# Optimization experiments

Hardware: AMD Instinct MI355X
Metric: run time of the kernel (lower is better)

The kernel has to match this reference:

```python
import jax, jax.numpy as jnp
import numpy as np

N_NODES = 50000

def _gcn_conv(x, W, b, src, dst, num_nodes):
    # PyG GCNConv: linear transform, then D^{-1/2} A_hat D^{-1/2} aggregation (A_hat has self-loops).
    xw = x @ W                                   # [N, out]
    ones = jnp.ones(src.shape[0], dtype=x.dtype)
    deg = jax.ops.segment_sum(ones, dst, num_segments=num_nodes)  # in-degree incl. self loop
    dinv = jnp.where(deg > 0, jax.lax.rsqrt(deg), 0.0)
    norm = dinv[src] * dinv[dst]                 # [E]
    msg = xw[src] * norm[:, None]                # [E, out] gather + scale
    out = jax.ops.segment_sum(msg, dst, num_segments=num_nodes)   # scatter-add
    return out + b

def _add_self_loops(edge_index, num_nodes):
    loop = jnp.arange(num_nodes, dtype=edge_index.dtype)
    src = jnp.concatenate([edge_index[0], loop])
    dst = jnp.concatenate([edge_index[1], loop])
    return src, dst

def setup_inputs() -> dict:
    key = jax.random.key(0)
    k = jax.random.split(key, 6)
    in_dim, hid_dim, out_dim = 256, 128, 64
    n_edges = 800000
    x = jax.random.normal(k[0], (N_NODES, in_dim), dtype=jnp.float32)
    edge_index = jax.random.randint(k[1], (2, n_edges), 0, N_NODES, dtype=jnp.int64)
    W1 = jax.random.normal(k[2], (in_dim, hid_dim), dtype=jnp.float32) / np.sqrt(in_dim)
    b1 = jnp.zeros((hid_dim,), dtype=jnp.float32)
    W2 = jax.random.normal(k[3], (hid_dim, out_dim), dtype=jnp.float32) / np.sqrt(hid_dim)
    b2 = jnp.zeros((out_dim,), dtype=jnp.float32)
    return {"x": x, "edge_index": edge_index, "W1": W1, "b1": b1, "W2": W2, "b2": b2}

def reference(x, edge_index, W1, b1, W2, b2):
    src, dst = _add_self_loops(edge_index, N_NODES)
    h = jnp.tanh(_gcn_conv(x, W1, b1, src, dst, N_NODES))
    out = _gcn_conv(h, W2, b2, src, dst, N_NODES)
    return out
```

## Files before the change

### kernel.cpp

```cpp
#include <hip/hip_runtime.h>

#define INDIM 256
#define HID 128
#define OUTD 64
#define BINSHIFT 8
#define MAXBIN 256

typedef _Float16 f16x8 __attribute__((ext_vector_type(8)));
typedef float    f32x4 __attribute__((ext_vector_type(4)));

__global__ __launch_bounds__(256) void k_hist_setup(const int* __restrict__ dst, int* __restrict__ bin_counts,
                                                    int E,
                                                    const float* __restrict__ W1, const float* __restrict__ W2,
                                                    _Float16* __restrict__ W1t, _Float16* __restrict__ W2t) {
    __shared__ int h[MAXBIN];
    int tid = threadIdx.x;
    h[tid] = 0;
    __syncthreads();
    int base = blockIdx.x * 4096;
#pragma unroll
    for (int i = 0; i < 16; i++) {
        int e = base + i * 256 + tid;
        if (e < E) atomicAdd(&h[dst[e] >> BINSHIFT], 1);
    }
    __syncthreads();
    int v = h[tid];
    if (v) atomicAdd(&bin_counts[tid], v);

    constexpr int NW1 = HID * INDIM;
    constexpr int NW2 = OUTD * HID;
    int id = blockIdx.x * 256 + tid;
    if (id < NW1) {
        int n = id / INDIM, k = id % INDIM;
        W1t[id] = (_Float16)W1[k * HID + n];
    } else if (id < NW1 + NW2) {
        int j = id - NW1;
        int n = j / HID, k = j % HID;
        W2t[j] = (_Float16)W2[k * OUTD + n];
    }
}

__global__ __launch_bounds__(256) void k_bscan(const int* __restrict__ bin_counts,
                                               int* __restrict__ bin_start, int* __restrict__ bin_cursor,
                                               int* __restrict__ row_start, int NBIN, int M, int E) {
    __shared__ int s[256];
    int tid = threadIdx.x;
    int v = (tid < NBIN) ? bin_counts[tid] : 0;
    s[tid] = v;
    __syncthreads();
#pragma unroll
    for (int off = 1; off < 256; off <<= 1) {
        int t = (tid >= off) ? s[tid - off] : 0;
        __syncthreads();
        s[tid] += t;
        __syncthreads();
    }
    if (tid < NBIN) {
        int excl = s[tid] - v;
        bin_start[tid] = excl;
        bin_cursor[tid] = excl;
    }
    if (tid == 0) {
        bin_start[NBIN] = E;
        row_start[M] = E;
    }
}

__global__ __launch_bounds__(256) void k_binfill(const int* __restrict__ src, const int* __restrict__ dst,
                                                 int* __restrict__ bin_cursor, int* __restrict__ binned, int E) {
    __shared__ int h[MAXBIN];
    __shared__ int rb[MAXBIN];
    int tid = threadIdx.x;
    h[tid] = 0;
    __syncthreads();
    int base = blockIdx.x * 2048;
    int ep[8], eb[8], rk[8];
#pragma unroll
    for (int i = 0; i < 8; i++) {
        int e = base + i * 256 + tid;
        if (e < E) {
            int s = src[e], d = dst[e];
            ep[i] = (s << 8) | (d & 255);
            eb[i] = d >> BINSHIFT;
            rk[i] = atomicAdd(&h[eb[i]], 1);
        } else {
            eb[i] = -1;
        }
    }
    __syncthreads();
    int c = h[tid];
    if (c) rb[tid] = atomicAdd(&bin_cursor[tid], c);
    __syncthreads();
#pragma unroll
    for (int i = 0; i < 8; i++) {
        if (eb[i] >= 0) binned[rb[eb[i]] + rk[i]] = ep[i];
    }
}

__global__ __launch_bounds__(256) void k_csr(const int* __restrict__ binned, const int* __restrict__ bin_start,
                                             int* __restrict__ row_start, float* __restrict__ dinv,
                                             int* __restrict__ edge_src, int M) {
    __shared__ int cnt[256];
    __shared__ int s[256];
    __shared__ int cur[256];
    int b = blockIdx.x, tid = threadIdx.x;
    int beg = bin_start[b], end = bin_start[b + 1];
    cnt[tid] = 0;
    __syncthreads();
    for (int i = beg + tid; i < end; i += 256) {
        atomicAdd(&cnt[binned[i] & 255], 1);
    }
    __syncthreads();
    int c = cnt[tid];
    s[tid] = c;
    __syncthreads();
#pragma unroll
    for (int off = 1; off < 256; off <<= 1) {
        int t = (tid >= off) ? s[tid - off] : 0;
        __syncthreads();
        s[tid] += t;
        __syncthreads();
    }
    int start = beg + s[tid] - c;
    int node = (b << BINSHIFT) + tid;
    if (node < M) {
        row_start[node] = start;
        dinv[node] = rsqrtf(1.0f + (float)c);
    }
    cur[tid] = start;
    __syncthreads();
    for (int i = beg + tid; i < end; i += 256) {
        int p = binned[i];
        int pos = atomicAdd(&cur[p & 255], 1);
        edge_src[pos] = p >> 8;
    }
}

template <int BN, int K, typename AT>
__global__ __launch_bounds__(256) void k_gemm_mfma(
    const AT* __restrict__ X, const _Float16* __restrict__ Wt,
    const float* __restrict__ dinv, _Float16* __restrict__ XW16, int M)
{
    constexpr int BM = 64;
    constexpr int BK = 32;
    constexpr int NT = BN / 16;
    constexpr int LDK = BK + 8;

    __shared__ __align__(16) _Float16 As[BM][LDK];
    __shared__ __align__(16) _Float16 Bs[BN][LDK];

    const int tid  = threadIdx.x;
    const int wave = tid >> 6;
    const int lane = tid & 63;
    const int m    = lane & 15;
    const int q    = lane >> 4;
    const int rb   = blockIdx.x * BM;

    f32x4 acc[NT];
#pragma unroll
    for (int t = 0; t < NT; t++) acc[t] = (f32x4){0.f, 0.f, 0.f, 0.f};

    for (int kt = 0; kt < K; kt += BK) {
        if (kt) __syncthreads();
        if constexpr (sizeof(AT) == 4) {
#pragma unroll
            for (int i = 0; i < BM * 8 / 256; i++) {
                int ch  = tid + i * 256;
                int row = ch >> 3;
                int c4  = ch & 7;
                int gr  = rb + row;
                float4 v = make_float4(0.f, 0.f, 0.f, 0.f);
                if (gr < M) v = *(const float4*)((const float*)X + (long)gr * K + kt + c4 * 4);
                _Float16* p = &As[row][c4 * 4];
                p[0] = (_Float16)v.x; p[1] = (_Float16)v.y;
                p[2] = (_Float16)v.z; p[3] = (_Float16)v.w;
            }
        } else {
            int row = tid >> 2;
            int c8  = tid & 3;
            int gr  = rb + row;
            uint4 v = make_uint4(0u, 0u, 0u, 0u);
            if (gr < M) v = *(const uint4*)((const _Float16*)X + (long)gr * K + kt + c8 * 8);
            *(uint4*)(&As[row][c8 * 8]) = v;
        }
#pragma unroll
        for (int i = 0; i < BN * 8 / 256; i++) {
            int ch = tid + i * 256;
            int n  = ch >> 3;
            int c4 = ch & 7;
            *(ushort4*)(&Bs[n][c4 * 4]) =
                *(const ushort4*)(Wt + (long)n * K + kt + c4 * 4);
        }
        __syncthreads();

        f16x8 af = *(const f16x8*)(&As[wave * 16 + m][q * 8]);
#pragma unroll
        for (int t = 0; t < NT; t++) {
            f16x8 bf = *(const f16x8*)(&Bs[t * 16 + m][q * 8]);
            acc[t] = __builtin_amdgcn_mfma_f32_16x16x32_f16(af, bf, acc[t], 0, 0, 0);
        }
    }

    int row0 = rb + wave * 16 + q * 4;
#pragma unroll
    for (int r = 0; r < 4; r++) {
        int row = row0 + r;
        if (row < M) {
            float di = dinv[row];
#pragma unroll
            for (int t = 0; t < NT; t++) {
                XW16[(long)row * BN + t * 16 + m] = (_Float16)(acc[t][r] * di);
            }
        }
    }
}

template <int F, bool TANH, typename OutT>
__global__ __launch_bounds__(256) void k_agg_csr(const int* __restrict__ row_start,
                                                 const int* __restrict__ edge_src,
                                                 const _Float16* __restrict__ feat,
                                                 const float* __restrict__ bias,
                                                 const float* __restrict__ dinv,
                                                 OutT* __restrict__ out, int M) {
    constexpr int LPN = F / 8;
    constexpr int NPB = 256 / LPN;
    int n = blockIdx.x * NPB + threadIdx.x / LPN;
    int c = threadIdx.x % LPN;
    if (n >= M) return;
    int beg = row_start[n], end = row_start[n + 1];

    f16x8 self = *(const f16x8*)(feat + (long)n * F + c * 8);
    float acc[8], acc2[8];
#pragma unroll
    for (int k = 0; k < 8; k++) { acc[k] = (float)self[k]; acc2[k] = 0.f; }

    int j = beg;
    for (; j + 3 < end; j += 4) {
        int s0 = edge_src[j],     s1 = edge_src[j + 1];
        int s2 = edge_src[j + 2], s3 = edge_src[j + 3];
        f16x8 v0 = *(const f16x8*)(feat + (long)s0 * F + c * 8);
        f16x8 v1 = *(const f16x8*)(feat + (long)s1 * F + c * 8);
        f16x8 v2 = *(const f16x8*)(feat + (long)s2 * F + c * 8);
        f16x8 v3 = *(const f16x8*)(feat + (long)s3 * F + c * 8);
#pragma unroll
        for (int k = 0; k < 8; k++) {
            acc[k]  += (float)v0[k] + (float)v1[k];
            acc2[k] += (float)v2[k] + (float)v3[k];
        }
    }
    for (; j < end; j++) {
        int s = edge_src[j];
        f16x8 v = *(const f16x8*)(feat + (long)s * F + c * 8);
#pragma unroll
        for (int k = 0; k < 8; k++) acc[k] += (float)v[k];
    }

    float di = dinv[n];
#pragma unroll
    for (int k = 0; k < 8; k++) acc[k] = bias[c * 8 + k] + di * (acc[k] + acc2[k]);
    if (TANH) {
#pragma unroll
        for (int k = 0; k < 8; k++) acc[k] = tanhf(acc[k]);
    }
    if constexpr (sizeof(OutT) == 2) {
        f16x8 o;
#pragma unroll
        for (int k = 0; k < 8; k++) o[k] = (_Float16)acc[k];
        __builtin_nontemporal_store(o, (f16x8*)((_Float16*)out + (long)n * F + c * 8));
    } else {
        f32x4 o0 = {acc[0], acc[1], acc[2], acc[3]};
        f32x4 o1 = {acc[4], acc[5], acc[6], acc[7]};
        float* p = (float*)out + (long)n * F + c * 8;
        __builtin_nontemporal_store(o0, (f32x4*)p);
        __builtin_nontemporal_store(o1, (f32x4*)(p + 4));
    }
}

extern "C" void kernel_launch(void* const* d_in, const int* in_sizes, int n_in,
                              void* d_out, int out_size, void* d_ws, size_t ws_size,
                              hipStream_t stream) {
    const float* x  = (const float*)d_in[0];
    const int*   ei = (const int*)d_in[1];
    const float* W1 = (const float*)d_in[2];
    const float* b1 = (const float*)d_in[3];
    const float* W2 = (const float*)d_in[4];
    const float* b2 = (const float*)d_in[5];
    float* out = (float*)d_out;

    const int M = in_sizes[0] / INDIM;
    const int E = in_sizes[1] / 2;
    const int* srcp = ei;
    const int* dstp = ei + E;

    const int Mp   = (M + 63) & ~63;
    const int NBIN = (M + 255) >> BINSHIFT;

    float*     dinv       = (float*)d_ws;
    int*       row_start  = (int*)(dinv + Mp);
    int*       bin_start  = row_start + Mp;
    int*       bin_cursor = bin_start + 258;
    int*       bin_counts = bin_cursor + MAXBIN;
    _Float16*  W1t        = (_Float16*)(bin_counts + MAXBIN);
    _Float16*  W2t        = W1t + HID * INDIM;
    int*       binned     = (int*)(W2t + OUTD * HID);
    int*       edge_src   = binned + E;
    _Float16*  xw16       = (_Float16*)(edge_src + E);
    _Float16*  h16        = xw16 + (long)M * HID;
    _Float16*  hw16       = xw16;

    const int NWH = (E + 4095) / 4096;
    const int NWF = (E + 2047) / 2048;

    hipMemsetAsync(bin_counts, 0, MAXBIN * sizeof(int), stream);
    k_hist_setup<<<NWH, 256, 0, stream>>>(dstp, bin_counts, E, W1, W2, W1t, W2t);
    k_bscan<<<1, 256, 0, stream>>>(bin_counts, bin_start, bin_cursor, row_start, NBIN, M, E);
    k_binfill<<<NWF, 256, 0, stream>>>(srcp, dstp, bin_cursor, binned, E);
    k_csr<<<NBIN, 256, 0, stream>>>(binned, bin_start, row_start, dinv, edge_src, M);

    k_gemm_mfma<HID, INDIM, float><<<(M + 63) / 64, 256, 0, stream>>>(x, W1t, dinv, xw16, M);
    k_agg_csr<HID, true, _Float16><<<(M + 15) / 16, 256, 0, stream>>>(row_start, edge_src, xw16, b1, dinv, h16, M);

    k_gemm_mfma<OUTD, HID, _Float16><<<(M + 63) / 64, 256, 0, stream>>>(h16, W2t, dinv, hw16, M);
    k_agg_csr<OUTD, false, float><<<(M + 31) / 32, 256, 0, stream>>>(row_start, edge_src, hw16, b2, dinv, out, M);
}
```

Baseline: 229.7 us.

## Fuse layer-1 aggregation with layer-2 GEMM and replace global histogram atomics

Layer-1 aggregation (with tanh) now writes its 64x128 tile of H into shared memory, and the same block runs the layer-2 MFMA GEMM on it. This removes the h16 round trip through global memory and one kernel launch. The global bin-count atomics and the memset are replaced by per-block partial histograms that the scan kernel sums serially. The fused kernel runs aggregation at 64 nodes per block, which lowers parallelism per block, and the scan now loops over roughly 200 partials per thread.

```diff
diff --git a/kernel.cpp b/kernel.cpp
--- a/kernel.cpp
+++ b/kernel.cpp
@@ -9,10 +9,10 @@
 typedef _Float16 f16x8 __attribute__((ext_vector_type(8)));
 typedef float    f32x4 __attribute__((ext_vector_type(4)));
 
-__global__ __launch_bounds__(256) void k_hist_setup(const int* __restrict__ dst, int* __restrict__ bin_counts,
-                                                    int E,
-                                                    const float* __restrict__ W1, const float* __restrict__ W2,
-                                                    _Float16* __restrict__ W1t, _Float16* __restrict__ W2t) {
+__global__ __launch_bounds__(256) void k_hist_prep(const int* __restrict__ dst, int* __restrict__ hist_part,
+                                                   int E,
+                                                   const float* __restrict__ W1, const float* __restrict__ W2,
+                                                   _Float16* __restrict__ W1t, _Float16* __restrict__ W2t) {
     __shared__ int h[MAXBIN];
     int tid = threadIdx.x;
     h[tid] = 0;
@@ -24,8 +24,7 @@
         if (e < E) atomicAdd(&h[dst[e] >> BINSHIFT], 1);
     }
     __syncthreads();
-    int v = h[tid];
-    if (v) atomicAdd(&bin_counts[tid], v);
+    hist_part[blockIdx.x * MAXBIN + tid] = h[tid];
 
     constexpr int NW1 = HID * INDIM;
     constexpr int NW2 = OUTD * HID;
@@ -40,12 +39,14 @@
     }
 }
 
-__global__ __launch_bounds__(256) void k_bscan(const int* __restrict__ bin_counts,
-                                               int* __restrict__ bin_start, int* __restrict__ bin_cursor,
-                                               int* __restrict__ row_start, int NBIN, int M, int E) {
+__global__ __launch_bounds__(256) void k_scan(const int* __restrict__ hist_part, int NWH,
+                                              int* __restrict__ bin_start, int* __restrict__ bin_cursor,
+                                              int* __restrict__ row_start, int NBIN, int M, int E) {
     __shared__ int s[256];
     int tid = threadIdx.x;
-    int v = (tid < NBIN) ? bin_counts[tid] : 0;
+    int v = 0;
+    for (int w = 0; w < NWH; w++) v += hist_part[w * MAXBIN + tid];
+    if (tid >= NBIN) v = 0;
     s[tid] = v;
     __syncthreads();
 #pragma unroll
@@ -136,13 +137,13 @@
     }
 }
 
-template <int BN, int K, typename AT>
-__global__ __launch_bounds__(256) void k_gemm_mfma(
-    const AT* __restrict__ X, const _Float16* __restrict__ Wt,
+__global__ __launch_bounds__(256) void k_gemm1(
+    const float* __restrict__ X, const _Float16* __restrict__ Wt,
     const float* __restrict__ dinv, _Float16* __restrict__ XW16, int M)
 {
     constexpr int BM = 64;
     constexpr int BK = 32;
+    constexpr int BN = HID;
     constexpr int NT = BN / 16;
     constexpr int LDK = BK + 8;
 
@@ -160,28 +161,19 @@
 #pragma unroll
     for (int t = 0; t < NT; t++) acc[t] = (f32x4){0.f, 0.f, 0.f, 0.f};
 
-    for (int kt = 0; kt < K; kt += BK) {
+    for (int kt = 0; kt < INDIM; kt += BK) {
         if (kt) __syncthreads();
-        if constexpr (sizeof(AT) == 4) {
-#pragma unroll
-            for (int i = 0; i < BM * 8 / 256; i++) {
-                int ch  = tid + i * 256;
-                int row = ch >> 3;
-                int c4  = ch & 7;
-                int gr  = rb + row;
-                float4 v = make_float4(0.f, 0.f, 0.f, 0.f);
-                if (gr < M) v = *(const float4*)((const float*)X + (long)gr * K + kt + c4 * 4);
-                _Float16* p = &As[row][c4 * 4];
-                p[0] = (_Float16)v.x; p[1] = (_Float16)v.y;
-                p[2] = (_Float16)v.z; p[3] = (_Float16)v.w;
-            }
-        } else {
-            int row = tid >> 2;
-            int c8  = tid & 3;
+#pragma unroll
+        for (int i = 0; i < BM * 8 / 256; i++) {
+            int ch  = tid + i * 256;
+            int row = ch >> 3;
+            int c4  = ch & 7;
             int gr  = rb + row;
-            uint4 v = make_uint4(0u, 0u, 0u, 0u);
-            if (gr < M) v = *(const uint4*)((const _Float16*)X + (long)gr * K + kt + c8 * 8);
-            *(uint4*)(&As[row][c8 * 8]) = v;
+            float4 v = make_float4(0.f, 0.f, 0.f, 0.f);
+            if (gr < M) v = *(const float4*)(X + (long)gr * INDIM + kt + c4 * 4);
+            _Float16* p = &As[row][c4 * 4];
+            p[0] = (_Float16)v.x; p[1] = (_Float16)v.y;
+            p[2] = (_Float16)v.z; p[3] = (_Float16)v.w;
         }
 #pragma unroll
         for (int i = 0; i < BN * 8 / 256; i++) {
@@ -189,7 +181,7 @@
             int n  = ch >> 3;
             int c4 = ch & 7;
             *(ushort4*)(&Bs[n][c4 * 4]) =
-                *(const ushort4*)(Wt + (long)n * K + kt + c4 * 4);
+                *(const ushort4*)(Wt + (long)n * INDIM + kt + c4 * 4);
         }
         __syncthreads();
 
@@ -215,16 +207,105 @@
     }
 }
 
-template <int F, bool TANH, typename OutT>
-__global__ __launch_bounds__(256) void k_agg_csr(const int* __restrict__ row_start,
-                                                 const int* __restrict__ edge_src,
-                                                 const _Float16* __restrict__ feat,
-                                                 const float* __restrict__ bias,
-                                                 const float* __restrict__ dinv,
-                                                 OutT* __restrict__ out, int M) {
+__global__ __launch_bounds__(256) void k_agg1_gemm2(
+    const int* __restrict__ row_start, const int* __restrict__ edge_src,
+    const _Float16* __restrict__ xw16, const float* __restrict__ b1,
+    const float* __restrict__ dinv, const _Float16* __restrict__ W2t,
+    _Float16* __restrict__ hw16, int M)
+{
+    constexpr int LDH = HID + 8;
+    __shared__ __align__(16) _Float16 Hs[64][LDH];
+
+    const int tid = threadIdx.x;
+    const int rb  = blockIdx.x * 64;
+
+#pragma unroll
+    for (int sub = 0; sub < 4; sub++) {
+        int nl = sub * 16 + (tid >> 4);
+        int n  = rb + nl;
+        int c  = tid & 15;
+        f16x8 o;
+        if (n < M) {
+            int beg = row_start[n], end = row_start[n + 1];
+            f16x8 self = *(const f16x8*)(xw16 + (long)n * HID + c * 8);
+            float acc[8], acc2[8];
+#pragma unroll
+            for (int k = 0; k < 8; k++) { acc[k] = (float)self[k]; acc2[k] = 0.f; }
+            int j = beg;
+            for (; j + 3 < end; j += 4) {
+                int s0 = edge_src[j],     s1 = edge_src[j + 1];
+                int s2 = edge_src[j + 2], s3 = edge_src[j + 3];
+                f16x8 v0 = *(const f16x8*)(xw16 + (long)s0 * HID + c * 8);
+                f16x8 v1 = *(const f16x8*)(xw16 + (long)s1 * HID + c * 8);
+                f16x8 v2 = *(const f16x8*)(xw16 + (long)s2 * HID + c * 8);
+                f16x8 v3 = *(const f16x8*)(xw16 + (long)s3 * HID + c * 8);
+#pragma unroll
+                for (int k = 0; k < 8; k++) {
+                    acc[k]  += (float)v0[k] + (float)v1[k];
+                    acc2[k] += (float)v2[k] + (float)v3[k];
+                }
+            }
+            for (; j < end; j++) {
+                int s = edge_src[j];
+                f16x8 v = *(const f16x8*)(xw16 + (long)s * HID + c * 8);
+#pragma unroll
+                for (int k = 0; k < 8; k++) acc[k] += (float)v[k];
+            }
+            float di = dinv[n];
+#pragma unroll
+            for (int k = 0; k < 8; k++)
+                o[k] = (_Float16)tanhf(b1[c * 8 + k] + di * (acc[k] + acc2[k]));
+        } else {
+#pragma unroll
+            for (int k = 0; k < 8; k++) o[k] = (_Float16)0.f;
+        }
+        *(f16x8*)(&Hs[nl][c * 8]) = o;
+    }
+    __syncthreads();
+
+    const int wave = tid >> 6;
+    const int lane = tid & 63;
+    const int m    = lane & 15;
+    const int q    = lane >> 4;
+    constexpr int NT = OUTD / 16;
+
+    f32x4 acc[NT];
+#pragma unroll
+    for (int t = 0; t < NT; t++) acc[t] = (f32x4){0.f, 0.f, 0.f, 0.f};
+
+#pragma unroll
+    for (int kt = 0; kt < HID; kt += 32) {
+        f16x8 af = *(const f16x8*)(&Hs[wave * 16 + m][kt + q * 8]);
+#pragma unroll
+        for (int t = 0; t < NT; t++) {
+            f16x8 bf = *(const f16x8*)(W2t + (long)(t * 16 + m) * HID + kt + q * 8);
+            acc[t] = __builtin_amdgcn_mfma_f32_16x16x32_f16(af, bf, acc[t], 0, 0, 0);
+        }
+    }
+
+    int row0 = rb + wave * 16 + q * 4;
+#pragma unroll
+    for (int r = 0; r < 4; r++) {
+        int row = row0 + r;
+        if (row < M) {
+            float di = dinv[row];
+#pragma unroll
+            for (int t = 0; t < NT; t++) {
+                hw16[(long)row * OUTD + t * 16 + m] = (_Float16)(acc[t][r] * di);
+            }
+        }
+    }
+}
+
+__global__ __launch_bounds__(256) void k_agg2(const int* __restrict__ row_start,
+                                              const int* __restrict__ edge_src,
+                                              const _Float16* __restrict__ feat,
+                                              const float* __restrict__ b2,
+                                              const float* __restrict__ dinv,
+                                              float* __restrict__ out, int M) {
+    constexpr int F = OUTD;
     constexpr int LPN = F / 8;
-    constexpr int NPB = 256 / LPN;
-    int n = blockIdx.x * NPB + threadIdx.x / LPN;
+    int n = blockIdx.x * (256 / LPN) + threadIdx.x / LPN;
     int c = threadIdx.x % LPN;
     if (n >= M) return;
     int beg = row_start[n], end = row_start[n + 1];
@@ -257,23 +338,13 @@
 
     float di = dinv[n];
 #pragma unroll
-    for (int k = 0; k < 8; k++) acc[k] = bias[c * 8 + k] + di * (acc[k] + acc2[k]);
-    if (TANH) {
-#pragma unroll
-        for (int k = 0; k < 8; k++) acc[k] = tanhf(acc[k]);
-    }
-    if constexpr (sizeof(OutT) == 2) {
-        f16x8 o;
-#pragma unroll
-        for (int k = 0; k < 8; k++) o[k] = (_Float16)acc[k];
-        __builtin_nontemporal_store(o, (f16x8*)((_Float16*)out + (long)n * F + c * 8));
-    } else {
-        f32x4 o0 = {acc[0], acc[1], acc[2], acc[3]};
-        f32x4 o1 = {acc[4], acc[5], acc[6], acc[7]};
-        float* p = (float*)out + (long)n * F + c * 8;
-        __builtin_nontemporal_store(o0, (f32x4*)p);
-        __builtin_nontemporal_store(o1, (f32x4*)(p + 4));
-    }
+    for (int k = 0; k < 8; k++) acc[k] = b2[c * 8 + k] + di * (acc[k] + acc2[k]);
+
+    f32x4 o0 = {acc[0], acc[1], acc[2], acc[3]};
+    f32x4 o1 = {acc[4], acc[5], acc[6], acc[7]};
+    float* p = out + (long)n * F + c * 8;
+    __builtin_nontemporal_store(o0, (f32x4*)p);
+    __builtin_nontemporal_store(o1, (f32x4*)(p + 4));
 }
 
 extern "C" void kernel_launch(void* const* d_in, const int* in_sizes, int n_in,
@@ -294,32 +365,30 @@
 
     const int Mp   = (M + 63) & ~63;
     const int NBIN = (M + 255) >> BINSHIFT;
+    int NWH = (E + 4095) / 4096;
+    if (NWH < 161) NWH = 161;
+    const int NWF = (E + 2047) / 2048;
 
     float*     dinv       = (float*)d_ws;
     int*       row_start  = (int*)(dinv + Mp);
     int*       bin_start  = row_start + Mp;
     int*       bin_cursor = bin_start + 258;
-    int*       bin_counts = bin_cursor + MAXBIN;
-    _Float16*  W1t        = (_Float16*)(bin_counts + MAXBIN);
+    int*       hist_part  = bin_cursor + MAXBIN;
+    _Float16*  W1t        = (_Float16*)(hist_part + (long)NWH * MAXBIN);
     _Float16*  W2t        = W1t + HID * INDIM;
     int*       binned     = (int*)(W2t + OUTD * HID);
     int*       edge_src   = binned + E;
     _Float16*  xw16       = (_Float16*)(edge_src + E);
-    _Float16*  h16        = xw16 + (long)M * HID;
-    _Float16*  hw16       = xw16;
-
-    const int NWH = (E + 4095) / 4096;
-    const int NWF = (E + 2047) / 2048;
-
-    hipMemsetAsync(bin_counts, 0, MAXBIN * sizeof(int), stream);
-    k_hist_setup<<<NWH, 256, 0, stream>>>(dstp, bin_counts, E, W1, W2, W1t, W2t);
-    k_bscan<<<1, 256, 0, stream>>>(bin_counts, bin_start, bin_cursor, row_start, NBIN, M, E);
+    _Float16*  hw16       = xw16 + (long)M * HID;
+
+    k_hist_prep<<<NWH, 256, 0, stream>>>(dstp, hist_part, E, W1, W2, W1t, W2t);
+    k_scan<<<1, 256, 0, stream>>>(hist_part, NWH, bin_start, bin_cursor, row_start, NBIN, M, E);
     k_binfill<<<NWF, 256, 0, stream>>>(srcp, dstp, bin_cursor, binned, E);
     k_csr<<<NBIN, 256, 0, stream>>>(binned, bin_start, row_start, dinv, edge_src, M);
 
-    k_gemm_mfma<HID, INDIM, float><<<(M + 63) / 64, 256, 0, stream>>>(x, W1t, dinv, xw16, M);
-    k_agg_csr<HID, true, _Float16><<<(M + 15) / 16, 256, 0, stream>>>(row_start, edge_src, xw16, b1, dinv, h16, M);
-
-    k_gemm_mfma<OUTD, HID, _Float16><<<(M + 63) / 64, 256, 0, stream>>>(h16, W2t, dinv, hw16, M);
-    k_agg_csr<OUTD, false, float><<<(M + 31) / 32, 256, 0, stream>>>(row_start, edge_src, hw16, b2, dinv, out, M);
-}
+    k_gemm1<<<(M + 63) / 64, 256, 0, stream>>>(x, W1t, dinv, xw16, M);
+
+    k_agg1_gemm2<<<(M + 63) / 64, 256, 0, stream>>>(row_start, edge_src, xw16, b1, dinv, W2t, hw16, M);
+
+    k_agg2<<<(M + 31) / 32, 256, 0, stream>>>(row_start, edge_src, hw16, b2, dinv, out, M);
+}
```

Result: slower. 253.6 us (+10.4%).
